# Performance work log

Hardware: AMD Instinct MI355X
Metric: run time of the kernel (lower is better)

## Reference

```python
import jax, jax.numpy as jnp
import numpy as np

N = 4096   # atoms
B = 64     # structures in batch
K = 128    # k-vectors per structure
E = 256    # emb_size_atom
D = 8      # downprojection_size
NUM_HIDDEN = 3


def _silu(x):
    return x * jax.nn.sigmoid(x)


def _residual(x, W):
    # ResidualLayer: two bias-free Dense(E,E) with SiLU, plus skip
    y = _silu(x @ W[0].T)
    y = _silu(y @ W[1].T)
    return x + y


def setup_inputs() -> dict:
    key = jax.random.key(0)
    ks = jax.random.split(key, 10)
    h = jax.random.normal(ks[0], (N, E), jnp.float32)
    x = jax.random.uniform(ks[1], (N, 3), jnp.float32) * 10.0  # Angstrom-scale positions
    k = jax.random.normal(ks[2], (B, K, 3), jnp.float32)
    batch_seg = jnp.sort(jax.random.randint(ks[3], (N,), 0, B))
    sc = 1.0 / np.sqrt(E)
    W_pre = jax.random.normal(ks[4], (2, E, E), jnp.float32) * sc        # pre_residual
    W_down = jax.random.normal(ks[5], (D, K), jnp.float32) / np.sqrt(K)  # shared downprojection (D,K)
    W_up = jax.random.normal(ks[6], (E, D), jnp.float32) / np.sqrt(D)    # up (E,D)
    W0 = jax.random.normal(ks[7], (E, E), jnp.float32) * sc              # first dense of ewald_layers
    W_res = jax.random.normal(ks[8], (NUM_HIDDEN, 2, E, E), jnp.float32) * sc
    return {"h": h, "x": x, "k": k, "batch_seg": batch_seg, "num_batch": B,
            "W_pre": W_pre, "W_down": W_down, "W_up": W_up, "W0": W0, "W_res": W_res}


def reference(h, x, k, batch_seg, num_batch, W_pre, W_down, W_up, W0, W_res):
    hres = _residual(h, W_pre)                       # (N,E)
    # dot products of atom positions with their structure's k-vectors
    dot = jnp.einsum('nkd,nd->nk', k[batch_seg], x)  # (N,K); sinc_damping == 1 (use_pbc)
    c, s = jnp.cos(dot), jnp.sin(dot)
    # structure factors: scatter-sum over atoms within each structure
    sf_real = jax.ops.segment_sum(hres[:, None, :] * c[:, :, None], batch_seg,
                                  num_segments=num_batch)  # (B,K,E)
    sf_imag = jax.ops.segment_sum(hres[:, None, :] * s[:, :, None], batch_seg,
                                  num_segments=num_batch)  # (B,K,E)
    # low-rank learned Fourier-space filter (use_pbc branch)
    kfilter = (W_up @ W_down).T                      # (K,E)
    # re-project filtered structure factors back to atoms
    h_update = 0.01 * jnp.sum(
        (sf_real * kfilter)[batch_seg] * c[:, :, None]
        + (sf_imag * kfilter)[batch_seg] * s[:, :, None], axis=1)  # (N,E)
    # ewald_layers update MLP: Dense + num_hidden residual blocks
    hu = _silu(h_update @ W0.T)
    for i in range(NUM_HIDDEN):
        hu = _residual(hu, W_res[i])
    return hu, dot
```

## Files before the change

kernel.cpp:

```cpp
#include <hip/hip_runtime.h>

#define NN 4096
#define BB 64
#define KK 128
#define EE 256
#define HTS 4352
#define CSR 4224
#define PCAP 160
#define YTS 264
#define ZTS 20

typedef unsigned short u16;
typedef __bf16 bhalf;
typedef bhalf bhalf8 __attribute__((ext_vector_type(8)));
typedef float floatx4 __attribute__((ext_vector_type(4)));

__device__ __forceinline__ float b2f(u16 u) {
  union { unsigned int i; float f; } v; v.i = ((unsigned int)u) << 16; return v.f;
}
__device__ __forceinline__ u16 f2b(float f) {
  union { float f; unsigned int i; } v; v.f = f;
  unsigned int r = (v.i + 0x7FFFu + ((v.i >> 16) & 1u)) >> 16;
  return (u16)r;
}
__device__ __forceinline__ float silu_f(float v) {
  return v / (1.f + __expf(-v));
}
__device__ __forceinline__ bhalf8 ld8f(const float* __restrict__ p) {
  float4 f0 = *(const float4*)p;
  float4 f1 = *(const float4*)(p + 4);
  union { bhalf8 v; u16 s[8]; } u;
  u.s[0] = f2b(f0.x); u.s[1] = f2b(f0.y); u.s[2] = f2b(f0.z); u.s[3] = f2b(f0.w);
  u.s[4] = f2b(f1.x); u.s[5] = f2b(f1.y); u.s[6] = f2b(f1.z); u.s[7] = f2b(f1.w);
  return u.v;
}


__global__ __launch_bounds__(256) void p1_k(
    const float* __restrict__ Wpre, const float* __restrict__ W0,
    const float* __restrict__ Wres, const float* __restrict__ Wup,
    const float* __restrict__ Wdn, const int* __restrict__ bs,
    const float* __restrict__ x, const float* __restrict__ kvec,
    u16* __restrict__ wpre, u16* __restrict__ w0b, u16* __restrict__ wrb,
    float* __restrict__ kft, u16* __restrict__ csb,
    int* __restrict__ seg, float* __restrict__ dout)
{
  int bid = blockIdx.x, tid = threadIdx.x;
  if (bid < 288) {
    int mat = bid >> 5;
    int w8 = ((bid & 31) * 256 + tid);
    int o = w8 * 8;
    int lane = w8 & 63, k = (w8 >> 6) & 7, nt = w8 >> 9;
    int r = lane & 15, q = lane >> 4;
    int src = (nt * 16 + r) * 256 + q * 8 + k * 32;
    const float* S; u16* D;
    if (mat < 2)      { S = Wpre + mat * 65536;       D = wpre + mat * 65536; }
    else if (mat == 2){ S = W0;                       D = w0b; }
    else              { S = Wres + (mat - 3) * 65536; D = wrb + (mat - 3) * 65536; }
    *(bhalf8*)(D + o) = ld8f(S + src);
  }
  else if (bid < 416) {
    int i = (bid - 288) * 256 + tid;
    int e = i >> 7, kk = i & 127;
    float a = 0.f;
#pragma unroll
    for (int d = 0; d < 8; ++d) a += Wup[e * 8 + d] * Wdn[d * KK + kk];
    kft[i] = a;
  } else if (bid < 424) {
    int base = 4096 * 256 + ((bid - 416) * 256 + tid) * 16;
    uint4 z = {0, 0, 0, 0};
    *(uint4*)(csb + base) = z;
    *(uint4*)(csb + base + 8) = z;
  } else if (bid == 424) {
    int b = tid;
    if (b <= BB) {
      int lo = 0, hi = NN;
      while (lo < hi) { int mid = (lo + hi) >> 1; if (bs[mid] < b) lo = mid + 1; else hi = mid; }
      seg[b] = lo;
    }
  } else {
    int i = (bid - 425) * 256 + tid;
    int n = i >> 7, kk = i & 127;
    int b = bs[n];
    const float* kp = kvec + (b * KK + kk) * 3;
    const float* xp = x + n * 3;
    float d = kp[0] * xp[0] + kp[1] * xp[1] + kp[2] * xp[2];
    float sv, cv;
    __sincosf(d, &sv, &cv);
    dout[i] = d;
    csb[(n << 8) + kk] = f2b(cv);
    csb[(n << 8) + 128 + kk] = f2b(sv);
  }
}

__global__ __launch_bounds__(256) void p2_k(
    const float* __restrict__ h, const u16* __restrict__ Wa, const u16* __restrict__ Wb,
    u16* __restrict__ ht,
    const u16* __restrict__ csb, const int* __restrict__ seg, u16* __restrict__ ctb)
{
  __shared__ u16 sh[8256];
  if (blockIdx.x < 256) {
    const int lane = threadIdx.x & 63, wv = threadIdx.x >> 6;
    const int m0 = blockIdx.x * 16;
    const int n0 = wv * 64;
    const int r = lane & 15, q = lane >> 4;
    const int lane8 = lane * 8;
    const float* Ap = h + (m0 + r) * EE + q * 8;
    floatx4 acc[4];
#pragma unroll
    for (int t = 0; t < 4; ++t) acc[t] = (floatx4){0.f, 0.f, 0.f, 0.f};
#pragma unroll
    for (int k = 0; k < 8; ++k) {
      bhalf8 av = ld8f(Ap + k * 32);
#pragma unroll
      for (int t = 0; t < 4; ++t) {
        bhalf8 bv = *(const bhalf8*)(Wa + ((wv * 4 + t) * 8 + k) * 512 + lane8);
        acc[t] = __builtin_amdgcn_mfma_f32_16x16x32_bf16(av, bv, acc[t], 0, 0, 0);
      }
    }
#pragma unroll
    for (int t = 0; t < 4; ++t) {
      int col = n0 + t * 16 + r;
#pragma unroll
      for (int i = 0; i < 4; ++i)
        sh[(q * 4 + i) * YTS + col] = f2b(silu_f(acc[t][i]));
    }
    __syncthreads();
#pragma unroll
    for (int t = 0; t < 4; ++t) acc[t] = (floatx4){0.f, 0.f, 0.f, 0.f};
#pragma unroll
    for (int k = 0; k < 8; ++k) {
      bhalf8 av = *(const bhalf8*)(&sh[r * YTS + q * 8 + k * 32]);
#pragma unroll
      for (int t = 0; t < 4; ++t) {
        bhalf8 bv = *(const bhalf8*)(Wb + ((wv * 4 + t) * 8 + k) * 512 + lane8);
        acc[t] = __builtin_amdgcn_mfma_f32_16x16x32_bf16(av, bv, acc[t], 0, 0, 0);
      }
    }
    __syncthreads();
#pragma unroll
    for (int t = 0; t < 4; ++t) {
      int col = n0 + t * 16 + r;
#pragma unroll
      for (int i = 0; i < 4; ++i) {
        int g = m0 + q * 4 + i;
        float v = silu_f(acc[t][i]) + h[g * EE + col];
        sh[col * ZTS + q * 4 + i] = f2b(v);
      }
    }
    __syncthreads();
    int e = threadIdx.x;
    const uint2* src = (const uint2*)&sh[e * ZTS];
    uint2* dst = (uint2*)(ht + e * HTS + m0);
#pragma unroll
    for (int i = 0; i < 4; ++i) dst[i] = src[i];
  } else {
    int bid2 = blockIdx.x - 256;
    int b = bid2 / 5, p0 = (bid2 % 5) * 32, t = threadIdx.x;
    int s0 = seg[b], s1 = seg[b + 1];
    int abase = s0 & ~7;
#pragma unroll
    for (int it = 0; it < 32; ++it) {
      int idx = it * 256 + t;
      int pl = idx >> 8, j = idx & 255;
      int n = abase + p0 + pl;
      u16 v = 0;
      if (n >= s0 && n < s1) v = csb[(n << 8) | j];
      sh[pl * 258 + j] = v;
    }
    __syncthreads();
    unsigned w[16];
#pragma unroll
    for (int i = 0; i < 16; ++i) {
      unsigned lo = sh[(2 * i) * 258 + t];
      unsigned hi = sh[(2 * i + 1) * 258 + t];
      w[i] = lo | (hi << 16);
    }
    uint4* dst = (uint4*)(ctb + ((b << 8) + t) * PCAP + p0);
#pragma unroll
    for (int i = 0; i < 4; ++i) {
      uint4 u; u.x = w[4*i]; u.y = w[4*i+1]; u.z = w[4*i+2]; u.w = w[4*i+3];
      dst[i] = u;
    }
  }
}

__global__ __launch_bounds__(256) void sf_k(
    const u16* __restrict__ ht, const u16* __restrict__ ctb,
    const float* __restrict__ kft, const int* __restrict__ seg, u16* __restrict__ F)
{
  const int lane = threadIdx.x & 63;
  const int wv = threadIdx.x >> 6;
  const int b = blockIdx.x;
  const int e0 = blockIdx.y * 128 + wv * 32;
  const int j0 = blockIdx.z * 64;
  const int r = lane & 15, q = lane >> 4;
  const int abase = seg[b] & ~7;
  const int phi = seg[b + 1] - abase;
  const u16* Ap = ht + (e0 + r) * HTS + abase + q * 8;
  const u16* Bp = ctb + ((b << 8) + j0 + r) * PCAP + q * 8;
  floatx4 acc[2][4];
#pragma unroll
  for (int m = 0; m < 2; ++m)
#pragma unroll
    for (int t = 0; t < 4; ++t) acc[m][t] = (floatx4){0.f, 0.f, 0.f, 0.f};
  for (int p0 = 0; p0 < phi; p0 += 32) {
    bhalf8 a0 = *(const bhalf8*)(Ap + p0);
    bhalf8 a1 = *(const bhalf8*)(Ap + 16 * HTS + p0);
#pragma unroll
    for (int t = 0; t < 4; ++t) {
      bhalf8 bv = *(const bhalf8*)(Bp + t * 16 * PCAP + p0);
      acc[0][t] = __builtin_amdgcn_mfma_f32_16x16x32_bf16(a0, bv, acc[0][t], 0, 0, 0);
      acc[1][t] = __builtin_amdgcn_mfma_f32_16x16x32_bf16(a1, bv, acc[1][t], 0, 0, 0);
    }
  }
#pragma unroll
  for (int m = 0; m < 2; ++m)
#pragma unroll
    for (int t = 0; t < 4; ++t) {
      int col = j0 + t * 16 + r;
      int kk = col & 127;
#pragma unroll
      for (int i = 0; i < 4; ++i) {
        int row = e0 + m * 16 + q * 4 + i;
        F[((b << 8) + row) * 256 + col] = f2b(acc[m][t][i] * kft[row * KK + kk]);
      }
    }
}

__device__ __forceinline__ void loadB(const u16* __restrict__ W, int wv, int lane8,
                                      bhalf8 (&bf)[8][2]) {
#pragma unroll
  for (int k = 0; k < 8; ++k)
#pragma unroll
    for (int t = 0; t < 2; ++t)
      bf[k][t] = *(const bhalf8*)(W + ((wv * 2 + t) * 8 + k) * 512 + lane8);
}

__device__ __forceinline__ void stageD(
    const u16* __restrict__ As, const bhalf8 (&B)[8][2],
    const u16* __restrict__ Wn, bhalf8 (&Bn)[8][2],
    u16* __restrict__ Ad, const u16* __restrict__ Ask,
    float* __restrict__ outg, int R0, int c0, int r, int q, int wv, int lane8)
{
  if (Wn) loadB(Wn, wv, lane8, Bn);
  bhalf8 a[8];
#pragma unroll
  for (int k = 0; k < 8; ++k)
    a[k] = *(const bhalf8*)(As + r * YTS + q * 8 + k * 32);
  floatx4 acc[2];
  acc[0] = (floatx4){0.f, 0.f, 0.f, 0.f};
  acc[1] = (floatx4){0.f, 0.f, 0.f, 0.f};
#pragma unroll
  for (int k = 0; k < 8; ++k) {
    acc[0] = __builtin_amdgcn_mfma_f32_16x16x32_bf16(a[k], B[k][0], acc[0], 0, 0, 0);
    acc[1] = __builtin_amdgcn_mfma_f32_16x16x32_bf16(a[k], B[k][1], acc[1], 0, 0, 0);
  }
#pragma unroll
  for (int t = 0; t < 2; ++t) {
    int col = c0 + t * 16 + r;
#pragma unroll
    for (int i = 0; i < 4; ++i) {
      int row = q * 4 + i;
      float v = silu_f(acc[t][i]);
      if (Ask) v += b2f(Ask[row * YTS + col]);
      if (outg) outg[(R0 + row) * EE + col] = v;
      else      Ad[row * YTS + col] = f2b(v);
    }
  }
}

__global__ __launch_bounds__(512) void tail_k(
    const u16* __restrict__ csb, const u16* __restrict__ F,
    const int* __restrict__ bs, const int* __restrict__ seg,
    const u16* __restrict__ w0b, const u16* __restrict__ wrb,
    float* __restrict__ out)
{
  __shared__ u16 A0[16 * YTS], A1[16 * YTS];
  const int R0 = blockIdx.x * 16;
  const int lane = threadIdx.x & 63, wv = threadIdx.x >> 6;
  const int r = lane & 15, q = lane >> 4;
  const int c0 = wv * 32;
  const int lane8 = lane * 8;
  bhalf8 B0[8][2], B1[8][2];
  {
    const u16* Ap = csb + (R0 + r) * 256 + q * 8;
    bhalf8 a[8];
#pragma unroll
    for (int k = 0; k < 8; ++k) a[k] = *(const bhalf8*)(Ap + k * 32);
    int s = bs[R0];
    while (true) {
      const u16* Bp = F + ((s << 8) + c0 + r) * 256 + q * 8;
      bhalf8 bf[8][2];
#pragma unroll
      for (int k = 0; k < 8; ++k) {
        bf[k][0] = *(const bhalf8*)(Bp + k * 32);
        bf[k][1] = *(const bhalf8*)(Bp + 16 * 256 + k * 32);
      }
      floatx4 acc[2];
      acc[0] = (floatx4){0.f, 0.f, 0.f, 0.f};
      acc[1] = (floatx4){0.f, 0.f, 0.f, 0.f};
#pragma unroll
      for (int k = 0; k < 8; ++k) {
        acc[0] = __builtin_amdgcn_mfma_f32_16x16x32_bf16(a[k], bf[k][0], acc[0], 0, 0, 0);
        acc[1] = __builtin_amdgcn_mfma_f32_16x16x32_bf16(a[k], bf[k][1], acc[1], 0, 0, 0);
      }
      int lo = seg[s] - R0;     if (lo < 0)  lo = 0;
      int hi = seg[s + 1] - R0; if (hi > 16) hi = 16;
#pragma unroll
      for (int t = 0; t < 2; ++t) {
        int col = c0 + t * 16 + r;
#pragma unroll
        for (int i = 0; i < 4; ++i) {
          int row = q * 4 + i;
          if (row >= lo && row < hi)
            A0[row * YTS + col] = f2b(0.01f * acc[t][i]);
        }
      }
      if (seg[s + 1] >= R0 + 16) break;
      ++s;
    }
  }
  loadB(w0b, wv, lane8, B0);
  __syncthreads();
  stageD(A0, B0, wrb + 0 * EE * EE, B1, A1, nullptr, nullptr, R0, c0, r, q, wv, lane8);
  __syncthreads();
  stageD(A1, B1, wrb + 1 * EE * EE, B0, A0, nullptr, nullptr, R0, c0, r, q, wv, lane8);
  __syncthreads();
  stageD(A0, B0, wrb + 2 * EE * EE, B1, A1, A1,      nullptr, R0, c0, r, q, wv, lane8);
  __syncthreads();
  stageD(A1, B1, wrb + 3 * EE * EE, B0, A0, nullptr, nullptr, R0, c0, r, q, wv, lane8);
  __syncthreads();
  stageD(A0, B0, wrb + 4 * EE * EE, B1, A1, A1,      nullptr, R0, c0, r, q, wv, lane8);
  __syncthreads();
  stageD(A1, B1, wrb + 5 * EE * EE, B0, A0, nullptr, nullptr, R0, c0, r, q, wv, lane8);
  __syncthreads();
  stageD(A0, B0, nullptr,           B1, nullptr, A1, out,     R0, c0, r, q, wv, lane8);
}

extern "C" void kernel_launch(void* const* d_in, const int* in_sizes, int n_in,
                              void* d_out, int out_size, void* d_ws, size_t ws_size,
                              hipStream_t stream) {
  const float* h    = (const float*)d_in[0];
  const float* x    = (const float*)d_in[1];
  const float* kv   = (const float*)d_in[2];
  const int*   bs   = (const int*)d_in[3];
  const float* Wpre = (const float*)d_in[5];
  const float* Wdn  = (const float*)d_in[6];
  const float* Wup  = (const float*)d_in[7];
  const float* W0   = (const float*)d_in[8];
  const float* Wres = (const float*)d_in[9];
  float* out = (float*)d_out;

  float* kft = (float*)d_ws;
  int*   seg = (int*)(kft + EE * KK);
  u16* wpre = (u16*)(seg + 128);
  u16* w0b  = wpre + 2 * EE * EE;
  u16* wrb  = w0b + EE * EE;
  u16* csb  = wrb + 6 * EE * EE;
  u16* ctb  = csb + CSR * 256;
  u16* ht   = ctb + BB * 256 * PCAP;
  u16* F    = ht + 256 * HTS;

  p1_k<<<2473, 256, 0, stream>>>(Wpre, W0, Wres, Wup, Wdn, bs, x, kv,
                                 wpre, w0b, wrb, kft, csb, seg, out + NN * EE);
  p2_k<<<576, 256, 0, stream>>>(h, wpre, wpre + EE * EE, ht, csb, seg, ctb);
  sf_k<<<dim3(BB, 2, 4), 256, 0, stream>>>(ht, ctb, kft, seg, F);
  tail_k<<<256, 512, 0, stream>>>(csb, F, bs, seg, w0b, wrb, out);
}
```

Baseline: 122.0 us.

## Fuse structure-factor GEMM into tail kernel, recomputing per row block

Removes the separate sf_k launch and the global F buffer. Each tail_k block now computes the filtered structure factors for its own segment(s) in 64-column chunks into shared memory, then immediately projects them back onto atoms. This saves one launch and the F write/read round trip. In exchange, every 16-row block recomputes the full per-structure GEMM over all atoms in that structure. With roughly 4 blocks per structure, that multiplies sf work several-fold, and the extra __syncthreads and shared memory may lower occupancy.

```diff
diff --git a/kernel.cpp b/kernel.cpp
--- a/kernel.cpp
+++ b/kernel.cpp
@@ -9,6 +9,7 @@
 #define PCAP 160
 #define YTS 264
 #define ZTS 20
+#define SFS 66
 
 typedef unsigned short u16;
 typedef __bf16 bhalf;
@@ -185,49 +186,6 @@
   }
 }
 
-__global__ __launch_bounds__(256) void sf_k(
-    const u16* __restrict__ ht, const u16* __restrict__ ctb,
-    const float* __restrict__ kft, const int* __restrict__ seg, u16* __restrict__ F)
-{
-  const int lane = threadIdx.x & 63;
-  const int wv = threadIdx.x >> 6;
-  const int b = blockIdx.x;
-  const int e0 = blockIdx.y * 128 + wv * 32;
-  const int j0 = blockIdx.z * 64;
-  const int r = lane & 15, q = lane >> 4;
-  const int abase = seg[b] & ~7;
-  const int phi = seg[b + 1] - abase;
-  const u16* Ap = ht + (e0 + r) * HTS + abase + q * 8;
-  const u16* Bp = ctb + ((b << 8) + j0 + r) * PCAP + q * 8;
-  floatx4 acc[2][4];
-#pragma unroll
-  for (int m = 0; m < 2; ++m)
-#pragma unroll
-    for (int t = 0; t < 4; ++t) acc[m][t] = (floatx4){0.f, 0.f, 0.f, 0.f};
-  for (int p0 = 0; p0 < phi; p0 += 32) {
-    bhalf8 a0 = *(const bhalf8*)(Ap + p0);
-    bhalf8 a1 = *(const bhalf8*)(Ap + 16 * HTS + p0);
-#pragma unroll
-    for (int t = 0; t < 4; ++t) {
-      bhalf8 bv = *(const bhalf8*)(Bp + t * 16 * PCAP + p0);
-      acc[0][t] = __builtin_amdgcn_mfma_f32_16x16x32_bf16(a0, bv, acc[0][t], 0, 0, 0);
-      acc[1][t] = __builtin_amdgcn_mfma_f32_16x16x32_bf16(a1, bv, acc[1][t], 0, 0, 0);
-    }
-  }
-#pragma unroll
-  for (int m = 0; m < 2; ++m)
-#pragma unroll
-    for (int t = 0; t < 4; ++t) {
-      int col = j0 + t * 16 + r;
-      int kk = col & 127;
-#pragma unroll
-      for (int i = 0; i < 4; ++i) {
-        int row = e0 + m * 16 + q * 4 + i;
-        F[((b << 8) + row) * 256 + col] = f2b(acc[m][t][i] * kft[row * KK + kk]);
-      }
-    }
-}
-
 __device__ __forceinline__ void loadB(const u16* __restrict__ W, int wv, int lane8,
                                       bhalf8 (&bf)[8][2]) {
 #pragma unroll
@@ -271,56 +229,96 @@
 }
 
 __global__ __launch_bounds__(512) void tail_k(
-    const u16* __restrict__ csb, const u16* __restrict__ F,
+    const u16* __restrict__ csb, const u16* __restrict__ ht,
+    const u16* __restrict__ ctb, const float* __restrict__ kft,
     const int* __restrict__ bs, const int* __restrict__ seg,
     const u16* __restrict__ w0b, const u16* __restrict__ wrb,
     float* __restrict__ out)
 {
+  __shared__ u16 SF[256 * SFS];
   __shared__ u16 A0[16 * YTS], A1[16 * YTS];
   const int R0 = blockIdx.x * 16;
   const int lane = threadIdx.x & 63, wv = threadIdx.x >> 6;
   const int r = lane & 15, q = lane >> 4;
   const int c0 = wv * 32;
+  const int e0w = wv * 32;
   const int lane8 = lane * 8;
+
+  int s = bs[R0];
+  while (true) {
+    const int abase = seg[s] & ~7;
+    const int phi = seg[s + 1] - abase;
+    floatx4 accu[2];
+    accu[0] = (floatx4){0.f, 0.f, 0.f, 0.f};
+    accu[1] = (floatx4){0.f, 0.f, 0.f, 0.f};
+#pragma unroll
+    for (int jq = 0; jq < 4; ++jq) {
+      const int j0 = jq * 64;
+      float kf[2][4][4];
+#pragma unroll
+      for (int m = 0; m < 2; ++m)
+#pragma unroll
+        for (int t = 0; t < 4; ++t) {
+          int kk = (j0 + t * 16 + r) & 127;
+#pragma unroll
+          for (int i = 0; i < 4; ++i)
+            kf[m][t][i] = kft[(e0w + m * 16 + q * 4 + i) * KK + kk];
+        }
+      bhalf8 au0 = *(const bhalf8*)(csb + (R0 + r) * 256 + j0 + q * 8);
+      bhalf8 au1 = *(const bhalf8*)(csb + (R0 + r) * 256 + j0 + q * 8 + 32);
+      {
+        const u16* Ap = ht + (e0w + r) * HTS + abase + q * 8;
+        const u16* Bp = ctb + ((s << 8) + j0 + r) * PCAP + q * 8;
+        floatx4 acc[2][4];
+#pragma unroll
+        for (int m = 0; m < 2; ++m)
+#pragma unroll
+          for (int t = 0; t < 4; ++t) acc[m][t] = (floatx4){0.f, 0.f, 0.f, 0.f};
+        for (int p0 = 0; p0 < phi; p0 += 32) {
+          bhalf8 a0 = *(const bhalf8*)(Ap + p0);
+          bhalf8 a1 = *(const bhalf8*)(Ap + 16 * HTS + p0);
+#pragma unroll
+          for (int t = 0; t < 4; ++t) {
+            bhalf8 bv = *(const bhalf8*)(Bp + t * 16 * PCAP + p0);
+            acc[0][t] = __builtin_amdgcn_mfma_f32_16x16x32_bf16(a0, bv, acc[0][t], 0, 0, 0);
+            acc[1][t] = __builtin_amdgcn_mfma_f32_16x16x32_bf16(a1, bv, acc[1][t], 0, 0, 0);
+          }
+        }
+#pragma unroll
+        for (int m = 0; m < 2; ++m)
+#pragma unroll
+          for (int t = 0; t < 4; ++t)
+#pragma unroll
+            for (int i = 0; i < 4; ++i)
+              SF[(e0w + m * 16 + q * 4 + i) * SFS + t * 16 + r] =
+                  f2b(acc[m][t][i] * kf[m][t][i]);
+      }
+      __syncthreads();
+#pragma unroll
+      for (int t = 0; t < 2; ++t) {
+        bhalf8 b0 = *(const bhalf8*)(&SF[(c0 + t * 16 + r) * SFS + q * 8]);
+        bhalf8 b1 = *(const bhalf8*)(&SF[(c0 + t * 16 + r) * SFS + q * 8 + 32]);
+        accu[t] = __builtin_amdgcn_mfma_f32_16x16x32_bf16(au0, b0, accu[t], 0, 0, 0);
+        accu[t] = __builtin_amdgcn_mfma_f32_16x16x32_bf16(au1, b1, accu[t], 0, 0, 0);
+      }
+      __syncthreads();
+    }
+    int lo = seg[s] - R0;     if (lo < 0)  lo = 0;
+    int hi = seg[s + 1] - R0; if (hi > 16) hi = 16;
+#pragma unroll
+    for (int t = 0; t < 2; ++t) {
+      int col = c0 + t * 16 + r;
+#pragma unroll
+      for (int i = 0; i < 4; ++i) {
+        int row = q * 4 + i;
+        if (row >= lo && row < hi)
+          A0[row * YTS + col] = f2b(0.01f * accu[t][i]);
+      }
+    }
+    if (seg[s + 1] >= R0 + 16) break;
+    ++s;
+  }
   bhalf8 B0[8][2], B1[8][2];
-  {
-    const u16* Ap = csb + (R0 + r) * 256 + q * 8;
-    bhalf8 a[8];
-#pragma unroll
-    for (int k = 0; k < 8; ++k) a[k] = *(const bhalf8*)(Ap + k * 32);
-    int s = bs[R0];
-    while (true) {
-      const u16* Bp = F + ((s << 8) + c0 + r) * 256 + q * 8;
-      bhalf8 bf[8][2];
-#pragma unroll
-      for (int k = 0; k < 8; ++k) {
-        bf[k][0] = *(const bhalf8*)(Bp + k * 32);
-        bf[k][1] = *(const bhalf8*)(Bp + 16 * 256 + k * 32);
-      }
-      floatx4 acc[2];
-      acc[0] = (floatx4){0.f, 0.f, 0.f, 0.f};
-      acc[1] = (floatx4){0.f, 0.f, 0.f, 0.f};
-#pragma unroll
-      for (int k = 0; k < 8; ++k) {
-        acc[0] = __builtin_amdgcn_mfma_f32_16x16x32_bf16(a[k], bf[k][0], acc[0], 0, 0, 0);
-        acc[1] = __builtin_amdgcn_mfma_f32_16x16x32_bf16(a[k], bf[k][1], acc[1], 0, 0, 0);
-      }
-      int lo = seg[s] - R0;     if (lo < 0)  lo = 0;
-      int hi = seg[s + 1] - R0; if (hi > 16) hi = 16;
-#pragma unroll
-      for (int t = 0; t < 2; ++t) {
-        int col = c0 + t * 16 + r;
-#pragma unroll
-        for (int i = 0; i < 4; ++i) {
-          int row = q * 4 + i;
-          if (row >= lo && row < hi)
-            A0[row * YTS + col] = f2b(0.01f * acc[t][i]);
-        }
-      }
-      if (seg[s + 1] >= R0 + 16) break;
-      ++s;
-    }
-  }
   loadB(w0b, wv, lane8, B0);
   __syncthreads();
   stageD(A0, B0, wrb + 0 * EE * EE, B1, A1, nullptr, nullptr, R0, c0, r, q, wv, lane8);
@@ -360,11 +358,9 @@
   u16* csb  = wrb + 6 * EE * EE;
   u16* ctb  = csb + CSR * 256;
   u16* ht   = ctb + BB * 256 * PCAP;
-  u16* F    = ht + 256 * HTS;
 
   p1_k<<<2473, 256, 0, stream>>>(Wpre, W0, Wres, Wup, Wdn, bs, x, kv,
                                  wpre, w0b, wrb, kft, csb, seg, out + NN * EE);
   p2_k<<<576, 256, 0, stream>>>(h, wpre, wpre + EE * EE, ht, csb, seg, ctb);
-  sf_k<<<dim3(BB, 2, 4), 256, 0, stream>>>(ht, ctb, kft, seg, F);
-  tail_k<<<256, 512, 0, stream>>>(csb, F, bs, seg, w0b, wrb, out);
-}
+  tail_k<<<256, 512, 0, stream>>>(csb, ht, ctb, kft, bs, seg, w0b, wrb, out);
+}
```

After: 138.5 us. 13.5% more time.
